# Kernel optimization log

Measured on AMD Instinct MI355X. Metric: run time of the kernel, lower is better.

The kernel has to match this reference:

```python
import jax, jax.numpy as jnp
import numpy as np


def setup_inputs() -> dict:
    key = jax.random.key(0)
    k1, k2 = jax.random.split(key)
    B, N, M, K = 8, 4096, 4096, 64
    input1 = jax.random.normal(k1, (B, N, K), dtype=jnp.float32)
    input2 = jax.random.normal(k2, (B, M, K), dtype=jnp.float32)
    return {"input1": input1, "input2": input2}


def reference(input1, input2):
    # Pairwise L2 distances via the ||x||^2 + ||y||^2 - 2<x,y> identity,
    # avoiding the O(B*N*M*K) broadcast-subtraction intermediate.
    x2 = jnp.sum(input1 * input1, axis=-1)                 # [B, N]
    y2 = jnp.sum(input2 * input2, axis=-1)                 # [B, M]
    xy = jnp.einsum('bnk,bmk->bnm', input1, input2)        # [B, N, M]
    sq = x2[:, :, None] + y2[:, None, :] - 2.0 * xy
    D = jnp.sqrt(jnp.maximum(sq, 0.0))                     # [B, N, M]
    dist0 = jnp.mean(jnp.min(D, axis=1), axis=1)           # min over N, mean over M
    dist1 = jnp.mean(jnp.min(D, axis=2), axis=1)           # min over M, mean over N
    loss = jnp.mean(dist0 + dist1)
    return loss
```

## Files before the change

### kernel.cpp

```cpp
#include <hip/hip_runtime.h>

#define BATCH 8
#define NPTS  4096
#define KD    64
#define FINF  3.0e38f

typedef float f32x4 __attribute__((ext_vector_type(4)));
typedef float f32x2 __attribute__((ext_vector_type(2)));
typedef short s16x8 __attribute__((ext_vector_type(8)));

__device__ __forceinline__ unsigned int f2bf(float f) {
  unsigned int u = __float_as_uint(f);
  u += 0x7FFFu + ((u >> 16) & 1u);
  return u >> 16;
}

__device__ __forceinline__ void stage16(const void* g, void* l) {
  __builtin_amdgcn_global_load_lds((const __attribute__((address_space(1))) void*)g,
                                   (__attribute__((address_space(3))) void*)l, 16, 0, 0);
}

__global__ __launch_bounds__(256)
void prep_kernel(const float* __restrict__ X, const float* __restrict__ Y,
                 unsigned int* __restrict__ Xbf, unsigned int* __restrict__ Ybf,
                 float* __restrict__ x2, float* __restrict__ y2) {
  int gid = blockIdx.x * 256 + threadIdx.x;
  int row = gid >> 5;
  int ki  = gid & 31;
  bool isX = row < BATCH * NPTS;
  int r2 = row & (BATCH * NPTS - 1);
  const float* src = isX ? X : Y;
  f32x2 v = *(const f32x2*)(src + (size_t)r2 * KD + ki * 2);
  float s = v[0] * v[0] + v[1] * v[1];
  #pragma unroll
  for (int m = 16; m >= 1; m >>= 1) s += __shfl_xor(s, m, 64);
  unsigned int packed = (f2bf(v[1]) << 16) | f2bf(v[0]);
  (isX ? Xbf : Ybf)[r2 * 32 + ki] = packed;
  if (ki == 0) (isX ? x2 : y2)[r2] = s;
}

__global__ __launch_bounds__(256, 2)
void chamfer_main(const unsigned short* __restrict__ Xbf,
                  const unsigned short* __restrict__ Ybf,
                  const float* __restrict__ x2g, const float* __restrict__ y2g,
                  float* __restrict__ rowpart,
                  float* __restrict__ colpart) {
  __shared__ __align__(16) unsigned short Xs[128 * 64];
  __shared__ __align__(16) unsigned short Ys[2][128 * 64];
  __shared__ float l_red[4 * 128];

  const int mhalf = blockIdx.x, ntile = blockIdx.y, b = blockIdx.z;
  const int n0 = ntile * 128;
  const int mbase = mhalf * 2048;
  const int t = threadIdx.x, w = t >> 6, lane = t & 63, c = lane & 15, q = lane >> 4;

  const int l8 = lane >> 3;
  const int lane_off = l8 * 128 + (((lane & 7) ^ l8) << 4);

  const char* Xg  = (const char*)(Xbf + (size_t)(b * NPTS + n0) * KD);
  const char* Yg0 = (const char*)(Ybf + (size_t)(b * NPTS + mbase) * KD);

  #pragma unroll
  for (int k = 0; k < 4; ++k) {
    int blockoff = (k * 32 + w * 8) * 128;
    int ldsoff   = (k * 256 + w * 64) * 16;
    stage16(Xg  + blockoff + lane_off, (char*)Xs    + ldsoff);
    stage16(Yg0 + blockoff + lane_off, (char*)Ys[0] + ldsoff);
  }

  f32x4 x2r[8];
  const float* x2b = x2g + b * NPTS + n0;
  #pragma unroll
  for (int i = 0; i < 8; ++i) x2r[i] = *(const f32x4*)(x2b + i * 16 + q * 4);

  __syncthreads();

  const int cx = c & 7;
  s16x8 xf[8][2];
  #pragma unroll
  for (int i = 0; i < 8; ++i)
    #pragma unroll
    for (int ks = 0; ks < 2; ++ks)
      xf[i][ks] = *(const s16x8*)&Xs[(i * 16 + c) * 64 + ((((ks << 2) + q) ^ cx) << 3)];

  float rm[8][4];
  #pragma unroll
  for (int i = 0; i < 8; ++i)
    #pragma unroll
    for (int r = 0; r < 4; ++r) rm[i][r] = FINF;

  const float* y2b = y2g + b * NPTS + mbase;
  float* colrow = colpart + (size_t)(ntile * 8 + b) * NPTS + mbase;
  const f32x4 zacc = {0.f, 0.f, 0.f, 0.f};

  #pragma unroll 2
  for (int tt = 0; tt < 16; ++tt) {
    unsigned short* cur = Ys[tt & 1];
    unsigned short* nb  = Ys[(tt + 1) & 1];
    if (tt < 15) {
      const char* Ygt = Yg0 + (size_t)(tt + 1) * 128 * 128;
      #pragma unroll
      for (int k = 0; k < 4; ++k)
        stage16(Ygt + (k * 32 + w * 8) * 128 + lane_off,
                (char*)nb + (k * 256 + w * 64) * 16);
    }
    float y2c0 = y2b[tt * 128 + w * 32 + c];
    float y2c1 = y2b[tt * 128 + w * 32 + 16 + c];

    s16x8 yf[2][2];
    #pragma unroll
    for (int j = 0; j < 2; ++j)
      #pragma unroll
      for (int ks = 0; ks < 2; ++ks)
        yf[j][ks] = *(const s16x8*)&cur[(w * 32 + j * 16 + c) * 64 +
                                        ((((ks << 2) + q) ^ cx) << 3)];

    f32x4 acc[8][2];
    #pragma unroll
    for (int i = 0; i < 8; ++i)
      #pragma unroll
      for (int j = 0; j < 2; ++j) {
        f32x4 a0 = __builtin_amdgcn_mfma_f32_16x16x32_bf16(xf[i][0], yf[j][0], zacc, 0, 0, 0);
        acc[i][j] = __builtin_amdgcn_mfma_f32_16x16x32_bf16(xf[i][1], yf[j][1], a0, 0, 0, 0);
      }

    float cm0 = FINF, cm1 = FINF;
    #pragma unroll
    for (int i = 0; i < 8; ++i)
      #pragma unroll
      for (int r = 0; r < 4; ++r) {
        float v0 = acc[i][0][r], v1 = acc[i][1][r];
        rm[i][r] = fminf(rm[i][r], fminf(fmaf(-2.f, v0, y2c0), fmaf(-2.f, v1, y2c1)));
        cm0 = fminf(cm0, fmaf(-2.f, v0, x2r[i][r]));
        cm1 = fminf(cm1, fmaf(-2.f, v1, x2r[i][r]));
      }
    cm0 = fminf(cm0, __shfl_xor(cm0, 16, 64));
    cm0 = fminf(cm0, __shfl_xor(cm0, 32, 64));
    cm1 = fminf(cm1, __shfl_xor(cm1, 16, 64));
    cm1 = fminf(cm1, __shfl_xor(cm1, 32, 64));
    if (q == 0)      colrow[tt * 128 + w * 32 + c]      = cm0 + y2c0;
    else if (q == 1) colrow[tt * 128 + w * 32 + 16 + c] = cm1 + y2c1;

    __syncthreads();
  }

  #pragma unroll
  for (int msk = 1; msk <= 8; msk <<= 1)
    #pragma unroll
    for (int i = 0; i < 8; ++i)
      #pragma unroll
      for (int r = 0; r < 4; ++r)
        rm[i][r] = fminf(rm[i][r], __shfl_xor(rm[i][r], msk, 64));
  {
    int ii = c >> 1, rb = (c & 1) * 2;
    l_red[w * 128 + ii * 16 + q * 4 + rb]     = rm[ii][rb];
    l_red[w * 128 + ii * 16 + q * 4 + rb + 1] = rm[ii][rb + 1];
  }
  __syncthreads();
  if (t < 128) {
    float v = fminf(fminf(l_red[t], l_red[128 + t]),
                    fminf(l_red[256 + t], l_red[384 + t]));
    rowpart[mhalf * (BATCH * NPTS) + b * NPTS + n0 + t] = v + x2b[t];
  }
}

__global__ __launch_bounds__(256)
void reduce_kernel(const float* __restrict__ rowpart, const float* __restrict__ colpart,
                   float* __restrict__ out) {
  int i = blockIdx.x * 256 + threadIdx.x;
  const int TOT = BATCH * NPTS;
  float rv = fminf(rowpart[i], rowpart[TOT + i]);
  float s = sqrtf(fmaxf(rv, 0.f));
  float cv = FINF;
  #pragma unroll
  for (int nt = 0; nt < 32; ++nt) cv = fminf(cv, colpart[nt * TOT + i]);
  s += sqrtf(fmaxf(cv, 0.f));
  #pragma unroll
  for (int m = 32; m >= 1; m >>= 1) s += __shfl_xor(s, m, 64);
  __shared__ float wsum[4];
  if ((threadIdx.x & 63) == 0) wsum[threadIdx.x >> 6] = s;
  __syncthreads();
  if (threadIdx.x == 0)
    atomicAdd(out, (wsum[0] + wsum[1] + wsum[2] + wsum[3]) * (1.0f / (float)TOT));
}

extern "C" void kernel_launch(void* const* d_in, const int* in_sizes, int n_in,
                              void* d_out, int out_size, void* d_ws, size_t ws_size,
                              hipStream_t stream) {
  const float* X = (const float*)d_in[0];
  const float* Y = (const float*)d_in[1];
  float* out = (float*)d_out;

  char* ws = (char*)d_ws;
  unsigned int* Xbf = (unsigned int*)ws;
  unsigned int* Ybf = (unsigned int*)(ws + (4u << 20));
  float* x2 = (float*)(ws + (8u << 20));
  float* y2 = (float*)(ws + (8u << 20) + (128u << 10));
  float* rowpart = (float*)(ws + (8u << 20) + (256u << 10));
  float* colpart = (float*)(ws + (8u << 20) + (512u << 10));

  hipMemsetAsync(out, 0, sizeof(float), stream);

  prep_kernel<<<dim3(2 * BATCH * NPTS * 32 / 256), dim3(256), 0, stream>>>(
      X, Y, Xbf, Ybf, x2, y2);

  chamfer_main<<<dim3(2, 32, 8), dim3(256), 0, stream>>>(
      (const unsigned short*)Xbf, (const unsigned short*)Ybf, x2, y2, rowpart, colpart);

  reduce_kernel<<<dim3(BATCH * NPTS / 256), dim3(256), 0, stream>>>(rowpart, colpart, out);
}
```

Baseline: 128.3 us.

## Split M dimension into eight chunks and process MFMA columns per j

Each block now covers 512 M columns instead of 2048, so the grid grows from 512 to 2048 blocks. The per-tile loop is fully unrolled over 4 tiles, and the MFMA and epilogue work is split per 16-column group to cut accumulator register pressure. Launch bounds are raised to allow 3 blocks per SM. The reduce kernel now takes the min over 8 row partials, which means more partial traffic and a larger workspace, and each block re-runs its X fragment setup more often.

Result: slower. 232.6 us (+81.2%).

```diff
diff --git a/kernel.cpp b/kernel.cpp
--- a/kernel.cpp
+++ b/kernel.cpp
@@ -3,6 +3,8 @@
 #define BATCH 8
 #define NPTS  4096
 #define KD    64
+#define MQ    8
+#define WALK  4
 #define FINF  3.0e38f
 
 typedef float f32x4 __attribute__((ext_vector_type(4)));
@@ -39,7 +41,7 @@
   if (ki == 0) (isX ? x2 : y2)[r2] = s;
 }
 
-__global__ __launch_bounds__(256, 2)
+__global__ __launch_bounds__(256, 3)
 void chamfer_main(const unsigned short* __restrict__ Xbf,
                   const unsigned short* __restrict__ Ybf,
                   const float* __restrict__ x2g, const float* __restrict__ y2g,
@@ -49,9 +51,9 @@
   __shared__ __align__(16) unsigned short Ys[2][128 * 64];
   __shared__ float l_red[4 * 128];
 
-  const int mhalf = blockIdx.x, ntile = blockIdx.y, b = blockIdx.z;
+  const int mq = blockIdx.x, ntile = blockIdx.y, b = blockIdx.z;
   const int n0 = ntile * 128;
-  const int mbase = mhalf * 2048;
+  const int mbase = mq * 512;
   const int t = threadIdx.x, w = t >> 6, lane = t & 63, c = lane & 15, q = lane >> 4;
 
   const int l8 = lane >> 3;
@@ -93,54 +95,45 @@
   float* colrow = colpart + (size_t)(ntile * 8 + b) * NPTS + mbase;
   const f32x4 zacc = {0.f, 0.f, 0.f, 0.f};
 
-  #pragma unroll 2
-  for (int tt = 0; tt < 16; ++tt) {
-    unsigned short* cur = Ys[tt & 1];
-    unsigned short* nb  = Ys[(tt + 1) & 1];
-    if (tt < 15) {
+  #pragma unroll
+  for (int tt = 0; tt < WALK; ++tt) {
+    const unsigned short* cur = Ys[tt & 1];
+    float y2c0 = y2b[tt * 128 + w * 32 + c];
+    float y2c1 = y2b[tt * 128 + w * 32 + 16 + c];
+
+    if (tt < WALK - 1) {
       const char* Ygt = Yg0 + (size_t)(tt + 1) * 128 * 128;
+      unsigned short* nb = Ys[(tt + 1) & 1];
       #pragma unroll
       for (int k = 0; k < 4; ++k)
         stage16(Ygt + (k * 32 + w * 8) * 128 + lane_off,
                 (char*)nb + (k * 256 + w * 64) * 16);
     }
-    float y2c0 = y2b[tt * 128 + w * 32 + c];
-    float y2c1 = y2b[tt * 128 + w * 32 + 16 + c];
-
-    s16x8 yf[2][2];
-    #pragma unroll
-    for (int j = 0; j < 2; ++j)
-      #pragma unroll
-      for (int ks = 0; ks < 2; ++ks)
-        yf[j][ks] = *(const s16x8*)&cur[(w * 32 + j * 16 + c) * 64 +
-                                        ((((ks << 2) + q) ^ cx) << 3)];
-
-    f32x4 acc[8][2];
-    #pragma unroll
-    for (int i = 0; i < 8; ++i)
-      #pragma unroll
-      for (int j = 0; j < 2; ++j) {
-        f32x4 a0 = __builtin_amdgcn_mfma_f32_16x16x32_bf16(xf[i][0], yf[j][0], zacc, 0, 0, 0);
-        acc[i][j] = __builtin_amdgcn_mfma_f32_16x16x32_bf16(xf[i][1], yf[j][1], a0, 0, 0, 0);
+
+    #pragma unroll
+    for (int j = 0; j < 2; ++j) {
+      s16x8 yf0 = *(const s16x8*)&cur[(w * 32 + j * 16 + c) * 64 + ((q ^ cx) << 3)];
+      s16x8 yf1 = *(const s16x8*)&cur[(w * 32 + j * 16 + c) * 64 + (((4 + q) ^ cx) << 3)];
+      f32x4 acc[8];
+      #pragma unroll
+      for (int i = 0; i < 8; ++i) {
+        f32x4 a0 = __builtin_amdgcn_mfma_f32_16x16x32_bf16(xf[i][0], yf0, zacc, 0, 0, 0);
+        acc[i] = __builtin_amdgcn_mfma_f32_16x16x32_bf16(xf[i][1], yf1, a0, 0, 0, 0);
       }
-
-    float cm0 = FINF, cm1 = FINF;
-    #pragma unroll
-    for (int i = 0; i < 8; ++i)
-      #pragma unroll
-      for (int r = 0; r < 4; ++r) {
-        float v0 = acc[i][0][r], v1 = acc[i][1][r];
-        rm[i][r] = fminf(rm[i][r], fminf(fmaf(-2.f, v0, y2c0), fmaf(-2.f, v1, y2c1)));
-        cm0 = fminf(cm0, fmaf(-2.f, v0, x2r[i][r]));
-        cm1 = fminf(cm1, fmaf(-2.f, v1, x2r[i][r]));
-      }
-    cm0 = fminf(cm0, __shfl_xor(cm0, 16, 64));
-    cm0 = fminf(cm0, __shfl_xor(cm0, 32, 64));
-    cm1 = fminf(cm1, __shfl_xor(cm1, 16, 64));
-    cm1 = fminf(cm1, __shfl_xor(cm1, 32, 64));
-    if (q == 0)      colrow[tt * 128 + w * 32 + c]      = cm0 + y2c0;
-    else if (q == 1) colrow[tt * 128 + w * 32 + 16 + c] = cm1 + y2c1;
-
+      float y2c = (j == 0) ? y2c0 : y2c1;
+      float cm = FINF;
+      #pragma unroll
+      for (int i = 0; i < 8; ++i)
+        #pragma unroll
+        for (int r = 0; r < 4; ++r) {
+          float v = acc[i][r];
+          rm[i][r] = fminf(rm[i][r], fmaf(-2.f, v, y2c));
+          cm = fminf(cm, fmaf(-2.f, v, x2r[i][r]));
+        }
+      cm = fminf(cm, __shfl_xor(cm, 16, 64));
+      cm = fminf(cm, __shfl_xor(cm, 32, 64));
+      if (q == j) colrow[tt * 128 + w * 32 + j * 16 + c] = cm + y2c;
+    }
     __syncthreads();
   }
 
@@ -160,7 +153,7 @@
   if (t < 128) {
     float v = fminf(fminf(l_red[t], l_red[128 + t]),
                     fminf(l_red[256 + t], l_red[384 + t]));
-    rowpart[mhalf * (BATCH * NPTS) + b * NPTS + n0 + t] = v + x2b[t];
+    rowpart[mq * (BATCH * NPTS) + b * NPTS + n0 + t] = v + x2b[t];
   }
 }
 
@@ -169,16 +162,18 @@
                    float* __restrict__ out) {
   int i = blockIdx.x * 256 + threadIdx.x;
   const int TOT = BATCH * NPTS;
-  float rv = fminf(rowpart[i], rowpart[TOT + i]);
-  float s = sqrtf(fmaxf(rv, 0.f));
+  float rv = FINF;
+  #pragma unroll
+  for (int s = 0; s < MQ; ++s) rv = fminf(rv, rowpart[s * TOT + i]);
+  float s0 = sqrtf(fmaxf(rv, 0.f));
   float cv = FINF;
   #pragma unroll
   for (int nt = 0; nt < 32; ++nt) cv = fminf(cv, colpart[nt * TOT + i]);
-  s += sqrtf(fmaxf(cv, 0.f));
-  #pragma unroll
-  for (int m = 32; m >= 1; m >>= 1) s += __shfl_xor(s, m, 64);
+  s0 += sqrtf(fmaxf(cv, 0.f));
+  #pragma unroll
+  for (int m = 32; m >= 1; m >>= 1) s0 += __shfl_xor(s0, m, 64);
   __shared__ float wsum[4];
-  if ((threadIdx.x & 63) == 0) wsum[threadIdx.x >> 6] = s;
+  if ((threadIdx.x & 63) == 0) wsum[threadIdx.x >> 6] = s0;
   __syncthreads();
   if (threadIdx.x == 0)
     atomicAdd(out, (wsum[0] + wsum[1] + wsum[2] + wsum[3]) * (1.0f / (float)TOT));
@@ -197,14 +192,14 @@
   float* x2 = (float*)(ws + (8u << 20));
   float* y2 = (float*)(ws + (8u << 20) + (128u << 10));
   float* rowpart = (float*)(ws + (8u << 20) + (256u << 10));
-  float* colpart = (float*)(ws + (8u << 20) + (512u << 10));
+  float* colpart = (float*)(ws + (9u << 20) + (256u << 10));
 
   hipMemsetAsync(out, 0, sizeof(float), stream);
 
   prep_kernel<<<dim3(2 * BATCH * NPTS * 32 / 256), dim3(256), 0, stream>>>(
       X, Y, Xbf, Ybf, x2, y2);
 
-  chamfer_main<<<dim3(2, 32, 8), dim3(256), 0, stream>>>(
+  chamfer_main<<<dim3(MQ, 32, 8), dim3(256), 0, stream>>>(
       (const unsigned short*)Xbf, (const unsigned short*)Ybf, x2, y2, rowpart, colpart);
 
   reduce_kernel<<<dim3(BATCH * NPTS / 256), dim3(256), 0, stream>>>(rowpart, colpart, out);
```
